# Optimization experiments

Hardware: AMD Instinct MI355X
Metric: run time of the kernel (lower is better)

Reference implementation:

```python
import jax, jax.numpy as jnp
import numpy as np

D = 1024        # hidden_size = input_size = output_size
E = 8           # num_experts
K = 2           # top-k
TEMP = 1.0      # router temperature


def setup_inputs() -> dict:
    key = jax.random.key(0)
    ks = jax.random.split(key, 7)
    s = 0.02
    x = jax.random.normal(ks[0], (4, 2048, D), dtype=jnp.float32)
    w_router = jax.random.normal(ks[1], (D, E), dtype=jnp.float32) * s
    w1 = jax.random.normal(ks[2], (E, D, D), dtype=jnp.float32) * s
    b1 = jnp.zeros((E, D), dtype=jnp.float32)
    w2 = jax.random.normal(ks[3], (E, D, D), dtype=jnp.float32) * s
    b2 = jnp.zeros((E, D), dtype=jnp.float32)
    return {"x": x, "w_router": w_router, "w1": w1, "b1": b1, "w2": w2, "b2": b2}


def reference(x, w_router, w1, b1, w2, b2):
    B, S, _ = x.shape
    # Router: temperature-scaled logits, softmax, top-k
    logits = jnp.einsum('bsd,de->bse', x, w_router) / TEMP          # [B,S,E]
    probs = jax.nn.softmax(logits, axis=-1)
    top_k_probs, top_k_idx = jax.lax.top_k(probs, K)                # [B,S,K]
    xt = x.reshape(-1, D)                                           # [T,D]
    idx = top_k_idx.reshape(-1, K)                                  # [T,K]
    pk = top_k_probs.reshape(-1, K)                                 # [T,K]
    # Dense expert eval: every expert on every token (faithful to source)
    h = jax.nn.gelu(jnp.einsum('td,edh->eth', xt, w1) + b1[:, None, :])
    expert_out = jnp.einsum('eth,ehd->etd', h, w2) + b2[:, None, :]  # [E,T,D]
    expert_out = jnp.transpose(expert_out, (1, 0, 2))                # [T,E,D]
    # Gather selected experts and combine with routing probs
    sel = jnp.take_along_axis(expert_out, idx[:, :, None], axis=1)   # [T,K,D]
    combined = jnp.sum(sel * pk[:, :, None], axis=1)                 # [T,D]
    return combined.reshape(B, S, D), logits
```

## Files before the change

### kernel.cpp

```cpp
#include <hip/hip_runtime.h>
#include <hip/hip_bf16.h>

#define DH 1024
#define NE 8
#define NT 8192
#define NTK 16384
#define BM 256
#define BN 256
#define BK 64
#define KT (DH / BK)

typedef __bf16 bf16x8 __attribute__((ext_vector_type(8)));
typedef float f32x4 __attribute__((ext_vector_type(4)));
typedef unsigned short u16;
typedef u16 u16x8 __attribute__((ext_vector_type(8)));
typedef u16 u16x4 __attribute__((ext_vector_type(4)));

__device__ __forceinline__ u16 f2bf(float f) {
  union { float f; unsigned u; } v; v.f = f;
  return (u16)((v.u + 0x7fffu + ((v.u >> 16) & 1u)) >> 16);
}
__device__ __forceinline__ float bf2f(u16 h) {
  union { unsigned u; float f; } v; v.u = ((unsigned)h) << 16;
  return v.f;
}
__device__ __forceinline__ float gelu_tanh(float v) {
  float y = 0.7978845608028654f * (v + 0.044715f * v * v * v);
  float t = 1.f - 2.f / (1.f + __expf(2.f * y));
  return 0.5f * v * (1.f + t);
}

__device__ __forceinline__ void gload_lds16(const u16* g, u16* l) {
  __builtin_amdgcn_global_load_lds(
      (const __attribute__((address_space(1))) void*)g,
      (__attribute__((address_space(3))) void*)l, 16, 0, 0);
}

__global__ __launch_bounds__(256) void prep_transpose(
    const float* __restrict__ w1, const float* __restrict__ w2,
    u16* __restrict__ w1t, u16* __restrict__ w2t) {
  __shared__ float tile[64][65];
  int z = blockIdx.z;
  const float* src = (z < NE) ? (w1 + (size_t)z * DH * DH) : (w2 + (size_t)(z - NE) * DH * DH);
  u16* dst = (z < NE) ? (w1t + (size_t)z * DH * DH) : (w2t + (size_t)(z - NE) * DH * DH);
  int d0 = blockIdx.y * 64, n0 = blockIdx.x * 64;
  int tid = threadIdx.x;
  int r16 = tid >> 4;
  int c4 = (tid & 15) * 4;
#pragma unroll
  for (int it = 0; it < 4; ++it) {
    int rr = it * 16 + r16;
    float4 v = *(const float4*)&src[(size_t)(d0 + rr) * DH + n0 + c4];
    tile[rr][c4] = v.x; tile[rr][c4 + 1] = v.y;
    tile[rr][c4 + 2] = v.z; tile[rr][c4 + 3] = v.w;
  }
  __syncthreads();
#pragma unroll
  for (int it = 0; it < 4; ++it) {
    int n = it * 16 + r16;
    u16x4 o;
    o[0] = f2bf(tile[c4][n]);     o[1] = f2bf(tile[c4 + 1][n]);
    o[2] = f2bf(tile[c4 + 2][n]); o[3] = f2bf(tile[c4 + 3][n]);
    *(u16x4*)&dst[(size_t)(n0 + n) * DH + d0 + c4] = o;
  }
}

__global__ __launch_bounds__(256) void router_kernel(
    const float* __restrict__ x, const float* __restrict__ wr,
    float* __restrict__ logits_out, int* __restrict__ tkidx,
    float* __restrict__ tkp, int* __restrict__ counts,
    u16* __restrict__ xb) {
  __shared__ float wsh[NE][DH + 8];
  __shared__ int hist[NE];
  int tid = threadIdx.x;
  for (int i = tid; i < DH * NE; i += 256) {
    int d = i >> 3, e = i & 7;
    wsh[e][d] = wr[i];
  }
  if (tid < NE) hist[tid] = 0;
  __syncthreads();

  int lane = tid & 63;
  int wv = tid >> 6;
  int t0 = blockIdx.x * 32 + wv * 8;
#pragma unroll 1
  for (int i = 0; i < 8; ++i) {
    int t = t0 + i;
    const float4* xp = (const float4*)(x + (size_t)t * DH);
    u16* xbrow = xb + (size_t)t * DH;
    float a[8] = {0.f, 0.f, 0.f, 0.f, 0.f, 0.f, 0.f, 0.f};
#pragma unroll
    for (int it = 0; it < 4; ++it) {
      float4 xv = xp[it * 64 + lane];
      int d0 = (it * 64 + lane) * 4;
      u16x4 c4;
      c4[0] = f2bf(xv.x); c4[1] = f2bf(xv.y); c4[2] = f2bf(xv.z); c4[3] = f2bf(xv.w);
      *(u16x4*)(xbrow + d0) = c4;
#pragma unroll
      for (int e = 0; e < 8; ++e) {
        float4 w4 = *(const float4*)&wsh[e][d0];
        a[e] += xv.x * w4.x + xv.y * w4.y + xv.z * w4.z + xv.w * w4.w;
      }
    }
#pragma unroll
    for (int off = 32; off; off >>= 1) {
#pragma unroll
      for (int e = 0; e < 8; ++e) a[e] += __shfl_xor(a[e], off, 64);
    }
    if (lane < 8) logits_out[(size_t)t * NE + lane] = a[lane];
    if (lane == 0) {
      float m1 = a[0]; int i1 = 0;
#pragma unroll
      for (int e = 1; e < 8; ++e) if (a[e] > m1) { m1 = a[e]; i1 = e; }
      float m2 = -3.4e38f; int i2 = 0;
#pragma unroll
      for (int e = 0; e < 8; ++e) if (e != i1 && a[e] > m2) { m2 = a[e]; i2 = e; }
      float den = 0.f;
#pragma unroll
      for (int e = 0; e < 8; ++e) den += expf(a[e] - m1);
      tkidx[2 * t] = i1; tkidx[2 * t + 1] = i2;
      tkp[2 * t] = 1.0f / den;
      tkp[2 * t + 1] = expf(m2 - m1) / den;
      atomicAdd(&hist[i1], 1);
      atomicAdd(&hist[i2], 1);
    }
  }
  __syncthreads();
  if (tid < NE) atomicAdd(&counts[tid], hist[tid]);
}

__global__ void offsets_kernel(const int* __restrict__ counts,
                               int* __restrict__ offs, int* __restrict__ cur,
                               int* __restrict__ tmap) {
  if (threadIdx.x == 0) {
    int s = 0;
    for (int e = 0; e < NE; ++e) { offs[e] = s; s += counts[e]; cur[e] = 0; }
    offs[NE] = s;
    int t = 0;
    for (int e = 0; e < NE; ++e)
      for (int m0 = 0; m0 < counts[e]; m0 += BM) {
        tmap[1 + 2 * t] = e; tmap[2 + 2 * t] = m0; ++t;
      }
    tmap[0] = t;
  }
}

__global__ __launch_bounds__(1024) void scatter_kernel(
    const int* __restrict__ tkidx, const float* __restrict__ tkp,
    const int* __restrict__ offs, int* __restrict__ cur,
    int* __restrict__ rows, int* __restrict__ posof, float* __restrict__ pp) {
  __shared__ int h[NE];
  __shared__ int base[NE];
  int tid = threadIdx.x;
  int gid = blockIdx.x * 1024 + tid;
  if (tid < NE) h[tid] = 0;
  __syncthreads();
  int e = tkidx[gid];
  int myrank = atomicAdd(&h[e], 1);
  __syncthreads();
  if (tid < NE) base[tid] = atomicAdd(&cur[tid], h[tid]);
  __syncthreads();
  int pos = offs[e] + base[e] + myrank;
  rows[pos] = gid >> 1;
  posof[gid] = pos;
  pp[pos] = tkp[gid];
}

template <int GELU>
__global__ __launch_bounds__(512, 2) void gemm_kernel(
    const u16* __restrict__ A, const u16* __restrict__ W,
    const float* __restrict__ bias, const int* __restrict__ counts,
    const int* __restrict__ offs, const int* __restrict__ rows,
    const int* __restrict__ tmap, u16* __restrict__ outb) {
  int ty = blockIdx.y;
  if (ty >= tmap[0]) return;
  int e = tmap[1 + 2 * ty];
  int m0 = tmap[2 + 2 * ty];
  int cnt = counts[e];
  int seg = offs[e];
  int n0 = blockIdx.x * BN;

  __shared__ __attribute__((aligned(16))) u16 lds[2][(BM + BN) * BK];

  int tid = threadIdx.x;
  int lane = tid & 63;
  int wv = tid >> 6;
  int wm = wv >> 2;
  int wn = wv & 3;

  int srow = tid >> 3;
  int schunk = ((tid & 7) ^ (srow & 7)) * 8;
  const u16* aSrc[4];
  const u16* bSrc[4];
#pragma unroll
  for (int i = 0; i < 4; ++i) {
    int gi = m0 + i * 64 + srow;
    int cl = gi < cnt ? gi : cnt - 1;
    int arow = GELU ? rows[seg + cl] : (seg + cl);
    aSrc[i] = A + (size_t)arow * DH + schunk;
    bSrc[i] = W + (size_t)e * DH * DH + (size_t)(n0 + i * 64 + srow) * DH + schunk;
  }

  auto stage = [&](int d, int k0) {
    u16* base = &lds[d][0];
#pragma unroll
    for (int i = 0; i < 4; ++i) {
      gload_lds16(aSrc[i] + k0, base + (i * 64 + wv * 8) * BK);
      gload_lds16(bSrc[i] + k0, base + BM * BK + (i * 64 + wv * 8) * BK);
    }
  };

  int lr = lane & 15;
  int quad = lane >> 4;
  int sx = lr & 7;
  int k0off = (quad ^ sx) * 8;
  int k1off = ((4 + quad) ^ sx) * 8;
  int wrr = wm * 128, wcc = wn * 64;

  f32x4 acc[8][4] = {};

  auto compute = [&](int d) {
    const u16* Ab = &lds[d][0];
    const u16* Bb = &lds[d][BM * BK];
    bf16x8 bfr[2][4];
#pragma unroll
    for (int n = 0; n < 4; ++n) {
      const u16* br = Bb + (size_t)(wcc + n * 16 + lr) * BK;
      bfr[0][n] = *(const bf16x8*)(br + k0off);
      bfr[1][n] = *(const bf16x8*)(br + k1off);
    }
#pragma unroll
    for (int s = 0; s < 4; ++s) {
      const u16* ar0 = Ab + (size_t)(wrr + (2 * s) * 16 + lr) * BK;
      const u16* ar1 = Ab + (size_t)(wrr + (2 * s + 1) * 16 + lr) * BK;
      bf16x8 a00 = *(const bf16x8*)(ar0 + k0off);
      bf16x8 a01 = *(const bf16x8*)(ar0 + k1off);
      bf16x8 a10 = *(const bf16x8*)(ar1 + k0off);
      bf16x8 a11 = *(const bf16x8*)(ar1 + k1off);
      __builtin_amdgcn_s_setprio(1);
#pragma unroll
      for (int n = 0; n < 4; ++n) {
        acc[2 * s][n]     = __builtin_amdgcn_mfma_f32_16x16x32_bf16(a00, bfr[0][n], acc[2 * s][n], 0, 0, 0);
        acc[2 * s][n]     = __builtin_amdgcn_mfma_f32_16x16x32_bf16(a01, bfr[1][n], acc[2 * s][n], 0, 0, 0);
        acc[2 * s + 1][n] = __builtin_amdgcn_mfma_f32_16x16x32_bf16(a10, bfr[0][n], acc[2 * s + 1][n], 0, 0, 0);
        acc[2 * s + 1][n] = __builtin_amdgcn_mfma_f32_16x16x32_bf16(a11, bfr[1][n], acc[2 * s + 1][n], 0, 0, 0);
      }
      __builtin_amdgcn_s_setprio(0);
    }
  };

  stage(0, 0);
  stage(1, BK);
#pragma unroll 1
  for (int t = 0; t < KT - 2; ++t) {
    asm volatile("s_waitcnt vmcnt(8)" ::: "memory");
    __builtin_amdgcn_s_barrier();
    asm volatile("" ::: "memory");
    compute(t & 1);
    asm volatile("" ::: "memory");
    __builtin_amdgcn_s_barrier();
    stage(t & 1, (t + 2) * BK);
  }
  asm volatile("s_waitcnt vmcnt(8)" ::: "memory");
  __builtin_amdgcn_s_barrier();
  asm volatile("" ::: "memory");
  compute((KT - 2) & 1);
  asm volatile("s_waitcnt vmcnt(0)" ::: "memory");
  __builtin_amdgcn_s_barrier();
  asm volatile("" ::: "memory");
  compute((KT - 1) & 1);

  int r4 = quad * 4;
  const float* be = bias + (size_t)e * DH;
#pragma unroll
  for (int m = 0; m < 8; ++m) {
#pragma unroll
    for (int n = 0; n < 4; ++n) {
      int col = n0 + wcc + n * 16 + lr;
      float bvv = be[col];
#pragma unroll
      for (int j = 0; j < 4; ++j) {
        int gr = m0 + wrr + m * 16 + r4 + j;
        if (gr < cnt) {
          float v = acc[m][n][j] + bvv;
          if (GELU) v = gelu_tanh(v);
          outb[(size_t)(seg + gr) * DH + col] = f2bf(v);
        }
      }
    }
  }
}

__global__ __launch_bounds__(256) void combine_kernel(
    const u16* __restrict__ eo, const float* __restrict__ tkp,
    const int* __restrict__ posof, float* __restrict__ out) {
  int gid = blockIdx.x * 256 + threadIdx.x;
  int t = gid >> 8;
  int n = (gid & 255) * 4;
  float p0 = tkp[2 * t], p1 = tkp[2 * t + 1];
  int q0 = posof[2 * t], q1 = posof[2 * t + 1];
  u16x4 a = *(const u16x4*)(eo + (size_t)q0 * DH + n);
  u16x4 b = *(const u16x4*)(eo + (size_t)q1 * DH + n);
  float4 o;
  o.x = p0 * bf2f(a[0]) + p1 * bf2f(b[0]);
  o.y = p0 * bf2f(a[1]) + p1 * bf2f(b[1]);
  o.z = p0 * bf2f(a[2]) + p1 * bf2f(b[2]);
  o.w = p0 * bf2f(a[3]) + p1 * bf2f(b[3]);
  *(float4*)(out + (size_t)t * DH + n) = o;
}

extern "C" void kernel_launch(void* const* d_in, const int* in_sizes, int n_in,
                              void* d_out, int out_size, void* d_ws, size_t ws_size,
                              hipStream_t stream) {
  const float* x = (const float*)d_in[0];
  const float* w_router = (const float*)d_in[1];
  const float* w1 = (const float*)d_in[2];
  const float* b1 = (const float*)d_in[3];
  const float* w2 = (const float*)d_in[4];
  const float* b2 = (const float*)d_in[5];
  float* out = (float*)d_out;
  float* logits = out + (size_t)NT * DH;

  char* ws = (char*)d_ws;
  size_t off = 0;
  auto alloc = [&](size_t bytes) -> void* {
    void* p = ws + off;
    off = (off + bytes + 255) & ~(size_t)255;
    return p;
  };
  int* ctrl = (int*)alloc(256);
  int* counts = ctrl;
  int* cur = ctrl + 8;
  int* offs = ctrl + 16;
  int* tmap = (int*)alloc(2048);
  int* tkidx = (int*)alloc((size_t)NTK * 4);
  float* tkp = (float*)alloc((size_t)NTK * 4);
  int* rows = (int*)alloc((size_t)NTK * 4);
  int* posof = (int*)alloc((size_t)NTK * 4);
  float* pp = (float*)alloc((size_t)NTK * 4);
  u16* w1t = (u16*)alloc((size_t)NE * DH * DH * 2);
  u16* w2t = (u16*)alloc((size_t)NE * DH * DH * 2);
  u16* hbuf = (u16*)alloc((size_t)NTK * DH * 2);
  u16* eo = (u16*)alloc((size_t)NTK * DH * 2);
  u16* xb = eo;

  hipMemsetAsync(ctrl, 0, 256, stream);

  prep_transpose<<<dim3(16, 16, 16), 256, 0, stream>>>(w1, w2, w1t, w2t);
  router_kernel<<<NT / 32, 256, 0, stream>>>(x, w_router, logits, tkidx, tkp, counts, xb);
  offsets_kernel<<<1, 64, 0, stream>>>(counts, offs, cur, tmap);
  scatter_kernel<<<NTK / 1024, 1024, 0, stream>>>(tkidx, tkp, offs, cur, rows, posof, pp);
  gemm_kernel<1><<<dim3(4, 72, 1), 512, 0, stream>>>(xb, w1t, b1, counts, offs, rows, tmap, hbuf);
  gemm_kernel<0><<<dim3(4, 72, 1), 512, 0, stream>>>(hbuf, w2t, b2, counts, offs, rows, tmap, eo);
  combine_kernel<<<NT, 256, 0, stream>>>(eo, tkp, posof, out);
}
```

Before: 224.6 us.

## Interleave global-to-LDS loads with MFMA phases in GEMM main loop

Restructures the GEMM K-loop so each 64-wide K step is split into four MFMA phases. Each phase issues one quarter of the next tile's global-to-LDS loads, reads fragments, and syncs with a barrier. The prefetch depth drops from two tiles ahead to one, with a full vmcnt(0) wait at every step. Launch bounds change from 2 to 1 waves per SIMD, which allows more registers at the cost of occupancy. The aim is finer-grained overlap of memory and matrix work, but the extra barriers and the shorter prefetch distance could expose more load latency.

Result: slower. 242.6 us (+8.0%).

```diff
diff --git a/kernel.cpp b/kernel.cpp
--- a/kernel.cpp
+++ b/kernel.cpp
@@ -167,7 +167,7 @@
 }
 
 template <int GELU>
-__global__ __launch_bounds__(512, 2) void gemm_kernel(
+__global__ __launch_bounds__(512, 1) void gemm_kernel(
     const u16* __restrict__ A, const u16* __restrict__ W,
     const float* __restrict__ bias, const int* __restrict__ counts,
     const int* __restrict__ offs, const int* __restrict__ rows,
@@ -201,12 +201,16 @@
     bSrc[i] = W + (size_t)e * DH * DH + (size_t)(n0 + i * 64 + srow) * DH + schunk;
   }
 
-  auto stage = [&](int d, int k0) {
+  auto stagePair = [&](int d, int k0, int j) {
     u16* base = &lds[d][0];
-#pragma unroll
-    for (int i = 0; i < 4; ++i) {
-      gload_lds16(aSrc[i] + k0, base + (i * 64 + wv * 8) * BK);
-      gload_lds16(bSrc[i] + k0, base + BM * BK + (i * 64 + wv * 8) * BK);
+    if (j < 2) {
+      int i0 = 2 * j;
+      gload_lds16(aSrc[i0] + k0, base + (i0 * 64 + wv * 8) * BK);
+      gload_lds16(aSrc[i0 + 1] + k0, base + ((i0 + 1) * 64 + wv * 8) * BK);
+    } else {
+      int i0 = 2 * (j - 2);
+      gload_lds16(bSrc[i0] + k0, base + BM * BK + (i0 * 64 + wv * 8) * BK);
+      gload_lds16(bSrc[i0 + 1] + k0, base + BM * BK + ((i0 + 1) * 64 + wv * 8) * BK);
     }
   };
 
@@ -219,56 +223,81 @@
 
   f32x4 acc[8][4] = {};
 
-  auto compute = [&](int d) {
+#pragma unroll
+  for (int j = 0; j < 4; ++j) stagePair(0, 0, j);
+
+#pragma unroll 1
+  for (int t = 0; t < KT; ++t) {
+    int d = t & 1;
     const u16* Ab = &lds[d][0];
     const u16* Bb = &lds[d][BM * BK];
-    bf16x8 bfr[2][4];
-#pragma unroll
-    for (int n = 0; n < 4; ++n) {
-      const u16* br = Bb + (size_t)(wcc + n * 16 + lr) * BK;
-      bfr[0][n] = *(const bf16x8*)(br + k0off);
-      bfr[1][n] = *(const bf16x8*)(br + k1off);
-    }
-#pragma unroll
-    for (int s = 0; s < 4; ++s) {
-      const u16* ar0 = Ab + (size_t)(wrr + (2 * s) * 16 + lr) * BK;
-      const u16* ar1 = Ab + (size_t)(wrr + (2 * s + 1) * 16 + lr) * BK;
-      bf16x8 a00 = *(const bf16x8*)(ar0 + k0off);
-      bf16x8 a01 = *(const bf16x8*)(ar0 + k1off);
-      bf16x8 a10 = *(const bf16x8*)(ar1 + k0off);
-      bf16x8 a11 = *(const bf16x8*)(ar1 + k1off);
-      __builtin_amdgcn_s_setprio(1);
-#pragma unroll
-      for (int n = 0; n < 4; ++n) {
-        acc[2 * s][n]     = __builtin_amdgcn_mfma_f32_16x16x32_bf16(a00, bfr[0][n], acc[2 * s][n], 0, 0, 0);
-        acc[2 * s][n]     = __builtin_amdgcn_mfma_f32_16x16x32_bf16(a01, bfr[1][n], acc[2 * s][n], 0, 0, 0);
-        acc[2 * s + 1][n] = __builtin_amdgcn_mfma_f32_16x16x32_bf16(a10, bfr[0][n], acc[2 * s + 1][n], 0, 0, 0);
-        acc[2 * s + 1][n] = __builtin_amdgcn_mfma_f32_16x16x32_bf16(a11, bfr[1][n], acc[2 * s + 1][n], 0, 0, 0);
-      }
-      __builtin_amdgcn_s_setprio(0);
-    }
-  };
-
-  stage(0, 0);
-  stage(1, BK);
-#pragma unroll 1
-  for (int t = 0; t < KT - 2; ++t) {
-    asm volatile("s_waitcnt vmcnt(8)" ::: "memory");
-    __builtin_amdgcn_s_barrier();
-    asm volatile("" ::: "memory");
-    compute(t & 1);
-    asm volatile("" ::: "memory");
-    __builtin_amdgcn_s_barrier();
-    stage(t & 1, (t + 2) * BK);
-  }
-  asm volatile("s_waitcnt vmcnt(8)" ::: "memory");
-  __builtin_amdgcn_s_barrier();
-  asm volatile("" ::: "memory");
-  compute((KT - 2) & 1);
-  asm volatile("s_waitcnt vmcnt(0)" ::: "memory");
-  __builtin_amdgcn_s_barrier();
-  asm volatile("" ::: "memory");
-  compute((KT - 1) & 1);
+    int nd = d ^ 1;
+    int nk = (t + 1) * BK;
+    bool st = (t + 1 < KT);
+
+    asm volatile("s_waitcnt vmcnt(0)" ::: "memory");
+    __builtin_amdgcn_s_barrier();
+
+    bf16x8 b0[4], b1[4], a[4];
+
+    if (st) stagePair(nd, nk, 0);
+#pragma unroll
+    for (int n = 0; n < 4; ++n)
+      b0[n] = *(const bf16x8*)(Bb + (size_t)(wcc + n * 16 + lr) * BK + k0off);
+#pragma unroll
+    for (int m = 0; m < 4; ++m)
+      a[m] = *(const bf16x8*)(Ab + (size_t)(wrr + m * 16 + lr) * BK + k0off);
+    __builtin_amdgcn_s_barrier();
+    __builtin_amdgcn_s_setprio(1);
+#pragma unroll
+    for (int m = 0; m < 4; ++m)
+#pragma unroll
+      for (int n = 0; n < 4; ++n)
+        acc[m][n] = __builtin_amdgcn_mfma_f32_16x16x32_bf16(a[m], b0[n], acc[m][n], 0, 0, 0);
+    __builtin_amdgcn_s_setprio(0);
+
+    if (st) stagePair(nd, nk, 1);
+#pragma unroll
+    for (int m = 0; m < 4; ++m)
+      a[m] = *(const bf16x8*)(Ab + (size_t)(wrr + (m + 4) * 16 + lr) * BK + k0off);
+    __builtin_amdgcn_s_barrier();
+    __builtin_amdgcn_s_setprio(1);
+#pragma unroll
+    for (int m = 0; m < 4; ++m)
+#pragma unroll
+      for (int n = 0; n < 4; ++n)
+        acc[m + 4][n] = __builtin_amdgcn_mfma_f32_16x16x32_bf16(a[m], b0[n], acc[m + 4][n], 0, 0, 0);
+    __builtin_amdgcn_s_setprio(0);
+
+    if (st) stagePair(nd, nk, 2);
+#pragma unroll
+    for (int n = 0; n < 4; ++n)
+      b1[n] = *(const bf16x8*)(Bb + (size_t)(wcc + n * 16 + lr) * BK + k1off);
+#pragma unroll
+    for (int m = 0; m < 4; ++m)
+      a[m] = *(const bf16x8*)(Ab + (size_t)(wrr + m * 16 + lr) * BK + k1off);
+    __builtin_amdgcn_s_barrier();
+    __builtin_amdgcn_s_setprio(1);
+#pragma unroll
+    for (int m = 0; m < 4; ++m)
+#pragma unroll
+      for (int n = 0; n < 4; ++n)
+        acc[m][n] = __builtin_amdgcn_mfma_f32_16x16x32_bf16(a[m], b1[n], acc[m][n], 0, 0, 0);
+    __builtin_amdgcn_s_setprio(0);
+
+    if (st) stagePair(nd, nk, 3);
+#pragma unroll
+    for (int m = 0; m < 4; ++m)
+      a[m] = *(const bf16x8*)(Ab + (size_t)(wrr + (m + 4) * 16 + lr) * BK + k1off);
+    __builtin_amdgcn_s_barrier();
+    __builtin_amdgcn_s_setprio(1);
+#pragma unroll
+    for (int m = 0; m < 4; ++m)
+#pragma unroll
+      for (int n = 0; n < 4; ++n)
+        acc[m + 4][n] = __builtin_amdgcn_mfma_f32_16x16x32_bf16(a[m], b1[n], acc[m + 4][n], 0, 0, 0);
+    __builtin_amdgcn_s_setprio(0);
+  }
 
   int r4 = quad * 4;
   const float* be = bias + (size_t)e * DH;
```

## Shrink expert GEMM tiles, triple-buffer K=32 stages, and remap workgroups across XCDs

Applied to the files above, without the earlier changes.

The expert GEMM's M tile is halved to 128 and the K step cut to 32, and LDS becomes a three-slot ring so two stages are always in flight. Launch bounds are raised to allow four blocks per CU. The grid grows to 136 tile rows, and block IDs are permuted so consecutive tiles land on the same XCD, aiming for better L2 reuse of expert weights. Smaller tiles should give finer load balance across uneven expert counts and more latency hiding. The cost is lower arithmetic intensity per tile, more barriers per K step, and tighter register pressure.

After: 196.2 us. -12.6%, faster.

```diff
diff --git a/kernel.cpp b/kernel.cpp
--- a/kernel.cpp
+++ b/kernel.cpp
@@ -5,10 +5,9 @@
 #define NE 8
 #define NT 8192
 #define NTK 16384
-#define BM 256
+#define BM 128
 #define BN 256
-#define BK 64
-#define KT (DH / BK)
+#define NSUB 32
 
 typedef __bf16 bf16x8 __attribute__((ext_vector_type(8)));
 typedef float f32x4 __attribute__((ext_vector_type(4)));
@@ -167,113 +166,87 @@
 }
 
 template <int GELU>
-__global__ __launch_bounds__(512, 2) void gemm_kernel(
+__global__ __launch_bounds__(512, 4) void gemm_kernel(
     const u16* __restrict__ A, const u16* __restrict__ W,
     const float* __restrict__ bias, const int* __restrict__ counts,
     const int* __restrict__ offs, const int* __restrict__ rows,
     const int* __restrict__ tmap, u16* __restrict__ outb) {
-  int ty = blockIdx.y;
+  int orig = blockIdx.y * 4 + blockIdx.x;
+  int wg = (orig & 7) * 68 + (orig >> 3);
+  int tx = wg & 3, ty = wg >> 2;
   if (ty >= tmap[0]) return;
   int e = tmap[1 + 2 * ty];
   int m0 = tmap[2 + 2 * ty];
   int cnt = counts[e];
   int seg = offs[e];
-  int n0 = blockIdx.x * BN;
-
-  __shared__ __attribute__((aligned(16))) u16 lds[2][(BM + BN) * BK];
+  int n0 = tx * BN;
+
+  __shared__ __attribute__((aligned(16))) u16 lds[3][12288];
 
   int tid = threadIdx.x;
   int lane = tid & 63;
   int wv = tid >> 6;
-  int wm = wv >> 2;
-  int wn = wv & 3;
-
-  int srow = tid >> 3;
-  int schunk = ((tid & 7) ^ (srow & 7)) * 8;
-  const u16* aSrc[4];
-  const u16* bSrc[4];
-#pragma unroll
-  for (int i = 0; i < 4; ++i) {
-    int gi = m0 + i * 64 + srow;
-    int cl = gi < cnt ? gi : cnt - 1;
-    int arow = GELU ? rows[seg + cl] : (seg + cl);
-    aSrc[i] = A + (size_t)arow * DH + schunk;
-    bSrc[i] = W + (size_t)e * DH * DH + (size_t)(n0 + i * 64 + srow) * DH + schunk;
-  }
-
-  auto stage = [&](int d, int k0) {
-    u16* base = &lds[d][0];
-#pragma unroll
-    for (int i = 0; i < 4; ++i) {
-      gload_lds16(aSrc[i] + k0, base + (i * 64 + wv * 8) * BK);
-      gload_lds16(bSrc[i] + k0, base + BM * BK + (i * 64 + wv * 8) * BK);
-    }
+
+  int srow = tid >> 2;
+  int sc8 = ((tid & 3) ^ ((srow >> 1) & 3)) * 8;
+  int gi = m0 + srow;
+  int cl = gi < cnt ? gi : cnt - 1;
+  int arow = GELU ? rows[seg + cl] : (seg + cl);
+  const u16* aSrc = A + (size_t)arow * DH + sc8;
+  const u16* bSrc0 = W + (size_t)e * DH * DH + (size_t)(n0 + srow) * DH + sc8;
+  const u16* bSrc1 = bSrc0 + (size_t)128 * DH;
+
+  int wb = wv * 512;
+  auto stage = [&](int slot, int s) {
+    int k0 = s * 32;
+    u16* base = &lds[slot][0];
+    gload_lds16(aSrc + k0, base + wb);
+    gload_lds16(bSrc0 + k0, base + 4096 + wb);
+    gload_lds16(bSrc1 + k0, base + 8192 + wb);
   };
 
   int lr = lane & 15;
   int quad = lane >> 4;
-  int sx = lr & 7;
-  int k0off = (quad ^ sx) * 8;
-  int k1off = ((4 + quad) ^ sx) * 8;
-  int wrr = wm * 128, wcc = wn * 64;
-
-  f32x4 acc[8][4] = {};
-
-  auto compute = [&](int d) {
-    const u16* Ab = &lds[d][0];
-    const u16* Bb = &lds[d][BM * BK];
-    bf16x8 bfr[2][4];
-#pragma unroll
-    for (int n = 0; n < 4; ++n) {
-      const u16* br = Bb + (size_t)(wcc + n * 16 + lr) * BK;
-      bfr[0][n] = *(const bf16x8*)(br + k0off);
-      bfr[1][n] = *(const bf16x8*)(br + k1off);
-    }
-#pragma unroll
-    for (int s = 0; s < 4; ++s) {
-      const u16* ar0 = Ab + (size_t)(wrr + (2 * s) * 16 + lr) * BK;
-      const u16* ar1 = Ab + (size_t)(wrr + (2 * s + 1) * 16 + lr) * BK;
-      bf16x8 a00 = *(const bf16x8*)(ar0 + k0off);
-      bf16x8 a01 = *(const bf16x8*)(ar0 + k1off);
-      bf16x8 a10 = *(const bf16x8*)(ar1 + k0off);
-      bf16x8 a11 = *(const bf16x8*)(ar1 + k1off);
-      __builtin_amdgcn_s_setprio(1);
-#pragma unroll
-      for (int n = 0; n < 4; ++n) {
-        acc[2 * s][n]     = __builtin_amdgcn_mfma_f32_16x16x32_bf16(a00, bfr[0][n], acc[2 * s][n], 0, 0, 0);
-        acc[2 * s][n]     = __builtin_amdgcn_mfma_f32_16x16x32_bf16(a01, bfr[1][n], acc[2 * s][n], 0, 0, 0);
-        acc[2 * s + 1][n] = __builtin_amdgcn_mfma_f32_16x16x32_bf16(a10, bfr[0][n], acc[2 * s + 1][n], 0, 0, 0);
-        acc[2 * s + 1][n] = __builtin_amdgcn_mfma_f32_16x16x32_bf16(a11, bfr[1][n], acc[2 * s + 1][n], 0, 0, 0);
-      }
-      __builtin_amdgcn_s_setprio(0);
-    }
-  };
+  int chunkOff = (quad ^ ((lr >> 1) & 3)) * 8;
+  int wm = wv >> 2, wn = wv & 3;
+  int wrr = wm * 64, wcc = wn * 64;
+
+  int aOff[4], bOff[4];
+#pragma unroll
+  for (int m = 0; m < 4; ++m) aOff[m] = (wrr + m * 16 + lr) * 32 + chunkOff;
+#pragma unroll
+  for (int n = 0; n < 4; ++n) bOff[n] = 4096 + (wcc + n * 16 + lr) * 32 + chunkOff;
+
+  f32x4 acc[4][4] = {};
 
   stage(0, 0);
-  stage(1, BK);
+  stage(1, 1);
+
 #pragma unroll 1
-  for (int t = 0; t < KT - 2; ++t) {
-    asm volatile("s_waitcnt vmcnt(8)" ::: "memory");
+  for (int s = 0; s < NSUB; ++s) {
+    if (s + 2 < NSUB) stage((s + 2) % 3, s + 2);
+    asm volatile("s_waitcnt vmcnt(6)" ::: "memory");
     __builtin_amdgcn_s_barrier();
-    asm volatile("" ::: "memory");
-    compute(t & 1);
-    asm volatile("" ::: "memory");
+    const u16* S = &lds[s % 3][0];
+    bf16x8 af[4], bf[4];
+#pragma unroll
+    for (int m = 0; m < 4; ++m) af[m] = *(const bf16x8*)(S + aOff[m]);
+#pragma unroll
+    for (int n = 0; n < 4; ++n) bf[n] = *(const bf16x8*)(S + bOff[n]);
+    __builtin_amdgcn_s_setprio(1);
+#pragma unroll
+    for (int m = 0; m < 4; ++m)
+#pragma unroll
+      for (int n = 0; n < 4; ++n)
+        acc[m][n] = __builtin_amdgcn_mfma_f32_16x16x32_bf16(af[m], bf[n], acc[m][n], 0, 0, 0);
+    __builtin_amdgcn_s_setprio(0);
     __builtin_amdgcn_s_barrier();
-    stage(t & 1, (t + 2) * BK);
-  }
-  asm volatile("s_waitcnt vmcnt(8)" ::: "memory");
-  __builtin_amdgcn_s_barrier();
-  asm volatile("" ::: "memory");
-  compute((KT - 2) & 1);
-  asm volatile("s_waitcnt vmcnt(0)" ::: "memory");
-  __builtin_amdgcn_s_barrier();
-  asm volatile("" ::: "memory");
-  compute((KT - 1) & 1);
+  }
 
   int r4 = quad * 4;
   const float* be = bias + (size_t)e * DH;
 #pragma unroll
-  for (int m = 0; m < 8; ++m) {
+  for (int m = 0; m < 4; ++m) {
 #pragma unroll
     for (int n = 0; n < 4; ++n) {
       int col = n0 + wcc + n * 16 + lr;
@@ -350,7 +323,7 @@
   router_kernel<<<NT / 32, 256, 0, stream>>>(x, w_router, logits, tkidx, tkp, counts, xb);
   offsets_kernel<<<1, 64, 0, stream>>>(counts, offs, cur, tmap);
   scatter_kernel<<<NTK / 1024, 1024, 0, stream>>>(tkidx, tkp, offs, cur, rows, posof, pp);
-  gemm_kernel<1><<<dim3(4, 72, 1), 512, 0, stream>>>(xb, w1t, b1, counts, offs, rows, tmap, hbuf);
-  gemm_kernel<0><<<dim3(4, 72, 1), 512, 0, stream>>>(hbuf, w2t, b2, counts, offs, rows, tmap, eo);
+  gemm_kernel<1><<<dim3(4, 136, 1), 512, 0, stream>>>(xb, w1t, b1, counts, offs, rows, tmap, hbuf);
+  gemm_kernel<0><<<dim3(4, 136, 1), 512, 0, stream>>>(hbuf, w2t, b2, counts, offs, rows, tmap, eo);
   combine_kernel<<<NT, 256, 0, stream>>>(eo, tkp, posof, out);
 }
```
